# Kernel optimization log

Hardware: AMD Instinct MI355X
Metric: run time of the kernel (lower is better)

The kernel has to match this reference:

```python
import jax, jax.numpy as jnp
import numpy as np

B, L, C, H, W = 2, 4, 128, 48, 176
RATIO, DS = 0.4, 4.0   # voxel_size[0], downsample_rate
NUM_ITER = 2


def _make_pairwise_t(key):
    k1, k2 = jax.random.split(key)
    theta = jax.random.uniform(k1, (B, L, L), minval=-0.2, maxval=0.2)
    t = jax.random.uniform(k2, (B, L, L, 2), minval=-8.0, maxval=8.0)  # meters
    c, s = jnp.cos(theta), jnp.sin(theta)
    T = jnp.zeros((B, L, L, 4, 4), dtype=jnp.float32)
    T = T.at[..., 0, 0].set(c).at[..., 0, 1].set(-s)
    T = T.at[..., 1, 0].set(s).at[..., 1, 1].set(c)
    T = T.at[..., 0, 3].set(t[..., 0]).at[..., 1, 3].set(t[..., 1])
    T = T.at[..., 2, 2].set(1.0).at[..., 3, 3].set(1.0)
    d = jnp.arange(L)
    T = T.at[:, d, d].set(jnp.eye(4, dtype=jnp.float32))  # self-transform = identity
    return T


def setup_inputs():
    key = jax.random.key(0)
    ks = jax.random.split(key, 8)
    x = jax.random.normal(ks[0], (B, L, C, H, W), dtype=jnp.float32)
    record_len = jnp.array([L, L - 1], dtype=jnp.int32)
    mask = (jnp.arange(L)[None, :] < record_len[:, None]).astype(jnp.float32)
    pairwise_t_matrix = _make_pairwise_t(ks[1])
    W_msg = jax.random.normal(ks[2], (C, 2 * C, 3, 3), dtype=jnp.float32) * 0.021
    b_msg = jnp.zeros((C,), dtype=jnp.float32)
    W_gates = jax.random.normal(ks[3], (2 * C, 3 * C, 3, 3), dtype=jnp.float32) * 0.017
    b_gates = jnp.zeros((2 * C,), dtype=jnp.float32)
    W_can = jax.random.normal(ks[4], (C, 3 * C, 3, 3), dtype=jnp.float32) * 0.017
    b_can = jnp.zeros((C,), dtype=jnp.float32)
    W_mlp = jax.random.normal(ks[5], (C, C), dtype=jnp.float32) * 0.088
    b_mlp = jnp.zeros((C,), dtype=jnp.float32)
    return {"x": x, "mask": mask, "pairwise_t_matrix": pairwise_t_matrix,
            "record_len": record_len, "W_msg": W_msg, "b_msg": b_msg,
            "W_gates": W_gates, "b_gates": b_gates, "W_can": W_can,
            "b_can": b_can, "W_mlp": W_mlp, "b_mlp": b_mlp}


def _conv2d(x, w, b):
    y = jax.lax.conv_general_dilated(x, w, (1, 1), 'SAME',
                                     dimension_numbers=('NCHW', 'OIHW', 'NCHW'))
    return y + b[None, :, None, None]


def _affine_inv(T):
    # T: (..., 4, 4) neighbor->ego transform. Returns (..., 2, 3) inverse pixel
    # affine (maps dst pixel -> src pixel), i.e. get_discretized_transformation_matrix
    # + rotation-about-center + translation, then inverted (kornia warp_affine semantics).
    R = T[..., :2, :2]
    t = T[..., :2, 3] / (RATIO * DS)             # translation in pixels
    c = jnp.array([W / 2.0, H / 2.0], dtype=T.dtype)
    full_t = c - jnp.einsum('...ij,j->...i', R, c) + t   # (..., 2)
    det = R[..., 0, 0] * R[..., 1, 1] - R[..., 0, 1] * R[..., 1, 0]
    Rinv = jnp.stack([jnp.stack([R[..., 1, 1], -R[..., 0, 1]], -1),
                      jnp.stack([-R[..., 1, 0], R[..., 0, 0]], -1)], -2) / det[..., None, None]
    tinv = -jnp.einsum('...ij,...j->...i', Rinv, full_t)
    return jnp.concatenate([Rinv, tinv[..., None]], axis=-1)


def _warp_one(img, A):
    # img: (C, H, W); A: (2, 3) dst->src pixel map. Bilinear, zeros padding.
    ys, xs = jnp.meshgrid(jnp.arange(H, dtype=img.dtype),
                          jnp.arange(W, dtype=img.dtype), indexing='ij')
    sx = A[0, 0] * xs + A[0, 1] * ys + A[0, 2]
    sy = A[1, 0] * xs + A[1, 1] * ys + A[1, 2]
    x0 = jnp.floor(sx); y0 = jnp.floor(sy)
    wx1 = sx - x0; wy1 = sy - y0
    def gather(xi, yi):
        valid = ((xi >= 0) & (xi <= W - 1) & (yi >= 0) & (yi <= H - 1)).astype(img.dtype)
        xc = jnp.clip(xi, 0, W - 1).astype(jnp.int32)
        yc = jnp.clip(yi, 0, H - 1).astype(jnp.int32)
        return img[:, yc, xc] * valid
    return (gather(x0, y0) * (1 - wx1) * (1 - wy1)
            + gather(x0 + 1, y0) * wx1 * (1 - wy1)
            + gather(x0, y0 + 1) * (1 - wx1) * wy1
            + gather(x0 + 1, y0 + 1) * wx1 * wy1)


def _forward(x, mask, pairwise_t_matrix, record_len,
             W_msg, b_msg, W_gates, b_gates, W_can, b_can, W_mlp, b_mlp):
    # Ainv[b, j, i] warps neighbor j into ego i's frame; reorder to (b, i, j).
    Ainv = _affine_inv(pairwise_t_matrix)                      # (B, L, L, 2, 3)
    Ainv_bij = jnp.transpose(Ainv, (0, 2, 1, 3, 4)).reshape(-1, 2, 3)
    warp_v = jax.vmap(_warp_one)
    ones_img = jnp.ones((1, H, W), dtype=x.dtype)
    roi = jax.vmap(lambda A: _warp_one(ones_img, A))(Ainv_bij)  # (B*L*L, 1, H, W)
    com_mask = roi.reshape(B, L, L, 1, H, W) * mask[:, None, :, None, None, None]
    rec = record_len.astype(x.dtype)[:, None, None, None, None]
    feat = x
    for _ in range(NUM_ITER):
        nb = jnp.broadcast_to(feat[:, None], (B, L, L, C, H, W)).reshape(-1, C, H, W)
        warped = warp_v(nb, Ainv_bij).reshape(B, L, L, C, H, W)
        ego = jnp.broadcast_to(feat[:, :, None], (B, L, L, C, H, W))
        msg_in = jnp.concatenate([warped, ego], axis=3).reshape(-1, 2 * C, H, W)
        msg = _conv2d(msg_in, W_msg, b_msg).reshape(B, L, L, C, H, W) * com_mask
        agg = jnp.sum(msg, axis=2) / rec                        # mean over N valid cavs
        # ConvGRU, single layer / single step, zero-initialized hidden state
        gru_in = jnp.concatenate([feat, agg], axis=2).reshape(-1, 2 * C, H, W)
        h = jnp.zeros((B * L, C, H, W), dtype=x.dtype)
        gates = jax.nn.sigmoid(_conv2d(jnp.concatenate([gru_in, h], 1), W_gates, b_gates))
        r, u = jnp.split(gates, 2, axis=1)
        cand = jnp.tanh(_conv2d(jnp.concatenate([gru_in, r * h], 1), W_can, b_can))
        h = (1 - u) * h + u * cand
        feat = h.reshape(B, L, C, H, W)
    out = feat[:, 0]                                            # ego agent of each sample
    return jnp.einsum('bchw,oc->bohw', out, W_mlp) + b_mlp[None, :, None, None]


def reference(x, mask, pairwise_t_matrix, record_len,
              W_msg, b_msg, W_gates, b_gates, W_can, b_can, W_mlp, b_mlp):
    return _forward(x, mask, pairwise_t_matrix, record_len,
                    W_msg, b_msg, W_gates, b_gates, W_can, b_can, W_mlp, b_mlp)
```

## Files before the change

kernel.cpp:

```cpp
#include <hip/hip_runtime.h>
#include <math.h>

#define BB 2
#define LL 4
#define CC 128
#define HH 48
#define WWID 176
#define HW 8448

typedef _Float16 f16;
typedef __attribute__((ext_vector_type(8))) _Float16 f16x8;
typedef __attribute__((ext_vector_type(4))) _Float16 f16x4;
typedef __attribute__((ext_vector_type(2))) _Float16 f16x2;
typedef __attribute__((ext_vector_type(4))) float f32x4;
typedef __attribute__((ext_vector_type(4))) unsigned int u32x4;

__device__ __forceinline__ void ainv_from(const float* __restrict__ t, float* a)
{
    float R00=t[0], R01=t[1], t0=t[3];
    float R10=t[4], R11=t[5], t1=t[7];
    float tx = t0 * 0.625f;
    float ty = t1 * 0.625f;
    const float cx = WWID/2.0f, cy = HH/2.0f;
    float ftx = cx - (R00*cx + R01*cy) + tx;
    float fty = cy - (R10*cx + R11*cy) + ty;
    float det = R00*R11 - R01*R10;
    float inv = 1.0f/det;
    float i00 =  R11*inv, i01 = -R01*inv, i10 = -R10*inv, i11 = R00*inv;
    a[0]=i00; a[1]=i01; a[2]=-(i00*ftx + i01*fty);
    a[3]=i10; a[4]=i11; a[5]=-(i10*ftx + i11*fty);
}

__global__ __launch_bounds__(256)
void prep_kernel(const float* __restrict__ Wm, const float* __restrict__ Wg,
                 const float* __restrict__ Wc, const float* __restrict__ x,
                 const float* __restrict__ T, const float* __restrict__ mask,
                 f16* __restrict__ WmF, f16* __restrict__ WuF, f16* __restrict__ WcF,
                 f16* __restrict__ xT, float* __restrict__ fac)
{
    int bid = blockIdx.x;
    int tid = threadIdx.x;
    if (bid < 3456) {
        int which = bid / 1152;
        const float* src = (which==0) ? Wm : (which==1) ? Wg : Wc;
        f16* dst         = (which==0) ? WmF : (which==1) ? WuF : WcF;
        int oc_off = (which==1) ? 128 : 0;
        int stride = (which==0) ? 256 : 384;
        int idx = (bid % 1152)*256 + tid;
        int j     = idx & 7;
        int hi    = (idx >> 3) & 3;
        int l15   = (idx >> 5) & 15;
        int ocblk = (idx >> 9) & 7;
        int kq    = (idx >> 12) & 7;
        int tap   = idx >> 15;
        int oc  = ocblk*16 + l15;
        int cin = kq*32 + hi*8 + j;
        dst[idx] = (f16)src[((size_t)(oc_off+oc)*stride + cin)*9 + tap];
    } else if (bid < 3720) {
        int g = bid - 3456;
        int bl = g / 33;
        int pix = (g % 33)*256 + tid;
        const float* src = x + (size_t)bl*CC*HW + pix;
        f16* dst = xT + (size_t)bl*HW*CC + (size_t)pix*CC;
        for (int gg = 0; gg < 8; ++gg) {
            f16x8 v0, v1;
            #pragma unroll
            for (int c2 = 0; c2 < 8; ++c2) {
                v0[c2] = (f16)src[(size_t)(gg*16 + c2    )*HW];
                v1[c2] = (f16)src[(size_t)(gg*16 + 8 + c2)*HW];
            }
            *(f16x8*)(dst + gg*16    ) = v0;
            *(f16x8*)(dst + gg*16 + 8) = v1;
        }
    } else {
        int g = bid - 3720;
        int slot = g / 33;
        int pix = (g % 33)*256 + tid;
        int b = slot >> 4, l2 = (slot >> 2) & 3;
        float mk = mask[b*LL + l2];
        float a[6];
        ainv_from(T + slot*16, a);
        float gx = (float)(pix % WWID), gy = (float)(pix / WWID);
        float sx = a[0]*gx + a[1]*gy + a[2];
        float sy = a[3]*gx + a[4]*gy + a[5];
        float x0 = floorf(sx), y0 = floorf(sy);
        float wx = sx-x0, wy = sy-y0;
        int xi=(int)x0, yi=(int)y0;
        bool vx0 = xi>=0 && xi<WWID, vx1 = xi+1>=0 && xi+1<WWID;
        bool vy0 = yi>=0 && yi<HH,   vy1 = yi+1>=0 && yi+1<HH;
        float r = (vx0&&vy0?(1.f-wx)*(1.f-wy):0.f) + (vx1&&vy0?wx*(1.f-wy):0.f)
                + (vx0&&vy1?(1.f-wx)*wy:0.f)       + (vx1&&vy1?wx*wy:0.f);
        fac[(size_t)slot*HW + pix] = r*mk;
    }
}

__global__ __launch_bounds__(256,3)
void msg_conv_kernel(const f16* __restrict__ featT, const float* __restrict__ T,
                     const float* __restrict__ fac, const float* __restrict__ mask,
                     const int* __restrict__ reclen,
                     const f16* __restrict__ WmF, const float* __restrict__ bm,
                     f16* __restrict__ Pm, int n_l1)
{
    int z = blockIdx.z;
    int b = z / (n_l1*5);
    int rem = z - b*(n_l1*5);
    int l1 = rem / 5, src = rem % 5;
    if (l1 != 0 && mask[b*LL + l1] == 0.f) return;
    bool ego = (src == 4);
    int l2 = ego ? l1 : src;
    if (!ego && mask[b*LL + l2] == 0.f) return;
    bool gather = (!ego) && (l2 != l1);

    int ty = blockIdx.x / 11, tx = blockIdx.x % 11;
    int y0 = ty*8, x0 = tx*16;
    int tid = threadIdx.x;
    int wid = tid >> 6, lane = tid & 63;
    int wr = wid >> 1, wc = wid & 1;
    int l15 = lane & 15, hi = lane >> 4;

    __shared__ short lt[180*128];
    __shared__ float tw[4][192];
    __shared__ int   tof[4][192];

    const f16* in = featT + (size_t)(b*LL + l2)*HW*CC;

    if (gather) {
        float a6[6];
        ainv_from(T + ((b*LL + l2)*LL + l1)*16, a6);
        float a0=a6[0],a1=a6[1],a2=a6[2],a3=a6[3],a4=a6[4],a5=a6[5];
        for (int r = tid; r < 180; r += 256) {
            int yy = r / 18, xx = r - yy*18;
            int gy = y0 - 1 + yy, gx = x0 - 1 + xx;
            float w00=0.f,w10=0.f,w01=0.f,w11=0.f;
            int o00=0,o10=0,o01=0,o11=0;
            if (gy>=0 && gy<HH && gx>=0 && gx<WWID) {
                float sx = a0*(float)gx + a1*(float)gy + a2;
                float sy = a3*(float)gx + a4*(float)gy + a5;
                float xf = floorf(sx), yf = floorf(sy);
                float wx = sx-xf, wyv = sy-yf;
                int xi=(int)xf, yi=(int)yf;
                bool vx0=xi>=0&&xi<WWID, vx1=xi+1>=0&&xi+1<WWID;
                bool vy0=yi>=0&&yi<HH,   vy1=yi+1>=0&&yi+1<HH;
                int xc0=min(max(xi,0),WWID-1), xc1=min(max(xi+1,0),WWID-1);
                int yc0=min(max(yi,0),HH-1),   yc1=min(max(yi+1,0),HH-1);
                o00=(yc0*WWID+xc0)*CC; o10=(yc0*WWID+xc1)*CC;
                o01=(yc1*WWID+xc0)*CC; o11=(yc1*WWID+xc1)*CC;
                w00=(vx0&&vy0)?(1.f-wx)*(1.f-wyv):0.f;
                w10=(vx1&&vy0)?wx*(1.f-wyv):0.f;
                w01=(vx0&&vy1)?(1.f-wx)*wyv:0.f;
                w11=(vx1&&vy1)?wx*wyv:0.f;
            }
            tw[0][r]=w00; tw[1][r]=w10; tw[2][r]=w01; tw[3][r]=w11;
            tof[0][r]=o00; tof[1][r]=o10; tof[2][r]=o01; tof[3][r]=o11;
        }
        __syncthreads();
        for (int i = tid; i < 180*16; i += 256) {
            int row = i >> 4, cg = i & 15;
            f16 h00=(f16)tw[0][row], h10=(f16)tw[1][row];
            f16 h01=(f16)tw[2][row], h11=(f16)tw[3][row];
            f16x2 W00={h00,h00}, W10={h10,h10}, W01={h01,h01}, W11={h11,h11};
            int o00=tof[0][row], o10=tof[1][row], o01=tof[2][row], o11=tof[3][row];
            f16x8 t00 = *(const f16x8*)(in + o00 + cg*8);
            f16x8 t10 = *(const f16x8*)(in + o10 + cg*8);
            f16x8 t01 = *(const f16x8*)(in + o01 + cg*8);
            f16x8 t11 = *(const f16x8*)(in + o11 + cg*8);
            const f16x2* p00 = (const f16x2*)&t00;
            const f16x2* p10 = (const f16x2*)&t10;
            const f16x2* p01 = (const f16x2*)&t01;
            const f16x2* p11 = (const f16x2*)&t11;
            f16x8 outv;
            f16x2* po = (f16x2*)&outv;
            #pragma unroll
            for (int q=0;q<4;++q)
                po[q] = p00[q]*W00 + p10[q]*W10 + p01[q]*W01 + p11[q]*W11;
            int byte = row*256 + ((cg*16) ^ ((row&7)<<4));
            *(f16x8*)((char*)lt + byte) = outv;
        }
    } else {
        for (int i = tid; i < 180*16; i += 256) {
            int row = i >> 4, cg = i & 15;
            int yy = row / 18, xx = row - yy*18;
            int gy = y0 - 1 + yy, gx = x0 - 1 + xx;
            u32x4 val = {0,0,0,0};
            if (gy>=0 && gy<HH && gx>=0 && gx<WWID)
                val = *(const u32x4*)(in + (size_t)(gy*WWID+gx)*CC + cg*8);
            int byte = row*256 + ((cg*16) ^ ((row&7)<<4));
            *(u32x4*)((char*)lt + byte) = val;
        }
    }
    __syncthreads();

    f32x4 acc[4][4];
    #pragma unroll
    for (int m=0;m<4;++m)
        #pragma unroll
        for (int n=0;n<4;++n) acc[m][n] = (f32x4){0.f,0.f,0.f,0.f};

    const int kqbase = ego ? 4 : 0;
    const f16* wlane = WmF + l15*32 + hi*8;
    __builtin_amdgcn_s_setprio(1);
    for (int tap=0; tap<9; ++tap) {
        int dy = tap/3, dx = tap - dy*3;
        #pragma unroll
        for (int kk=0; kk<4; ++kk) {
            const f16* wt = wlane + (size_t)(((tap*8 + kqbase + kk)*8 + wr*4))*512;
            f16x8 av[4];
            #pragma unroll
            for (int m=0;m<4;++m)
                av[m] = *(const f16x8*)(wt + m*512);
            f16x8 bv[4];
            #pragma unroll
            for (int n=0;n<4;++n) {
                int pos = (wc*4 + n + dy)*18 + dx + l15;
                int byte = pos*256 + ((kk*64 + hi*16) ^ ((pos&7)<<4));
                bv[n] = *(const f16x8*)((const char*)lt + byte);
            }
            #pragma unroll
            for (int m=0;m<4;++m)
                #pragma unroll
                for (int n=0;n<4;++n)
                    acc[m][n] = __builtin_amdgcn_mfma_f32_16x16x32_f16(
                        av[m], bv[n], acc[m][n], 0, 0, 0);
        }
    }
    __builtin_amdgcn_s_setprio(0);

    float invrec = 1.0f / (float)reclen[b];
    float fsc[4];
    if (ego) {
        #pragma unroll
        for (int n=0;n<4;++n) fsc[n] = 0.f;
        for (int j=0;j<LL;++j) {
            if (mask[b*LL + j] == 0.f) continue;
            const float* fp = fac + (size_t)(b*16 + j*4 + l1)*HW;
            #pragma unroll
            for (int n=0;n<4;++n)
                fsc[n] += fp[(y0 + wc*4 + n)*WWID + x0 + l15];
        }
    } else {
        const float* fp = fac + (size_t)(b*16 + l2*4 + l1)*HW;
        #pragma unroll
        for (int n=0;n<4;++n)
            fsc[n] = fp[(y0 + wc*4 + n)*WWID + x0 + l15];
    }
    #pragma unroll
    for (int n=0;n<4;++n) fsc[n] *= invrec;

    f16* outp = Pm + (size_t)z*HW*CC;
    #pragma unroll
    for (int m=0;m<4;++m) {
        f32x4 b4 = {0.f,0.f,0.f,0.f};
        if (ego) b4 = *(const f32x4*)(bm + wr*64 + m*16 + hi*4);
        #pragma unroll
        for (int n=0;n<4;++n) {
            int pix = (y0 + wc*4 + n)*WWID + x0 + l15;
            int oc  = wr*64 + m*16 + hi*4;
            f32x4 v = (acc[m][n] + b4) * fsc[n];
            f16x4 h = {(f16)v[0], (f16)v[1], (f16)v[2], (f16)v[3]};
            *(f16x4*)(outp + (size_t)pix*CC + oc) = h;
        }
    }
}

__global__ __launch_bounds__(256)
void reduce_agg_kernel(const f16* __restrict__ Pm, const float* __restrict__ mask,
                       f16* __restrict__ aggT, int n_l1)
{
    int zi = blockIdx.y;
    int b = zi / n_l1, l1 = zi % n_l1;
    if (l1 != 0 && mask[b*LL + l1] == 0.f) return;
    int pix = blockIdx.x*256 + threadIdx.x;
    bool act[4];
    #pragma unroll
    for (int j=0;j<LL;++j) act[j] = (mask[b*LL + j] != 0.f);
    const f16* base = Pm + (size_t)(zi*5)*HW*CC + (size_t)pix*CC;
    f16* dst = aggT + (size_t)zi*HW*CC + (size_t)pix*CC;
    for (int cg=0; cg<16; ++cg) {
        float s[8];
        f16x8 e = *(const f16x8*)(base + (size_t)4*HW*CC + cg*8);
        #pragma unroll
        for (int j8=0;j8<8;++j8) s[j8] = (float)e[j8];
        #pragma unroll
        for (int j=0;j<4;++j) {
            if (!act[j]) continue;
            f16x8 p = *(const f16x8*)(base + (size_t)j*HW*CC + cg*8);
            #pragma unroll
            for (int j8=0;j8<8;++j8) s[j8] += (float)p[j8];
        }
        f16x8 o;
        #pragma unroll
        for (int j8=0;j8<8;++j8) o[j8] = (f16)s[j8];
        *(f16x8*)(dst + cg*8) = o;
    }
}

__global__ __launch_bounds__(256,3)
void gru_conv_kernel(const f16* __restrict__ featT, const f16* __restrict__ aggT,
                     const float* __restrict__ mask,
                     const f16* __restrict__ WuF, const f16* __restrict__ WcF,
                     f16* __restrict__ Pg, int n_l1)
{
    int z = blockIdx.z;
    int b = z / n_l1, l1 = z % n_l1;
    if (l1 != 0 && mask[b*LL + l1] == 0.f) return;
    int gate = blockIdx.y;

    int ty = blockIdx.x / 11, tx = blockIdx.x % 11;
    int y0 = ty*8, x0 = tx*16;
    int tid = threadIdx.x;
    int wid = tid >> 6, lane = tid & 63;
    int wr = wid >> 1, wc = wid & 1;
    int l15 = lane & 15, hi = lane >> 4;

    __shared__ short lt[180*128];

    f32x4 acc[4][4];
    #pragma unroll
    for (int m=0;m<4;++m)
        #pragma unroll
        for (int n=0;n<4;++n) acc[m][n] = (f32x4){0.f,0.f,0.f,0.f};

    const f16* WF = (gate==0) ? WuF : WcF;
    const f16* wlane = WF + l15*32 + hi*8;

    for (int s = 0; s < 2; ++s) {
        const f16* in = (s==0) ? featT + (size_t)(b*LL + l1)*HW*CC
                               : aggT  + (size_t)(b*n_l1 + l1)*HW*CC;
        if (s) __syncthreads();
        for (int i = tid; i < 180*16; i += 256) {
            int row = i >> 4, cg = i & 15;
            int yy = row / 18, xx = row - yy*18;
            int gy = y0 - 1 + yy, gx = x0 - 1 + xx;
            u32x4 val = {0,0,0,0};
            if (gy>=0 && gy<HH && gx>=0 && gx<WWID)
                val = *(const u32x4*)(in + (size_t)(gy*WWID+gx)*CC + cg*8);
            int byte = row*256 + ((cg*16) ^ ((row&7)<<4));
            *(u32x4*)((char*)lt + byte) = val;
        }
        __syncthreads();

        int kqbase = s*4;
        __builtin_amdgcn_s_setprio(1);
        for (int tap=0; tap<9; ++tap) {
            int dy = tap/3, dx = tap - dy*3;
            #pragma unroll
            for (int kk=0; kk<4; ++kk) {
                const f16* wt = wlane + (size_t)(((tap*8 + kqbase + kk)*8 + wr*4))*512;
                f16x8 av[4];
                #pragma unroll
                for (int m=0;m<4;++m)
                    av[m] = *(const f16x8*)(wt + m*512);
                f16x8 bv[4];
                #pragma unroll
                for (int n=0;n<4;++n) {
                    int pos = (wc*4 + n + dy)*18 + dx + l15;
                    int byte = pos*256 + ((kk*64 + hi*16) ^ ((pos&7)<<4));
                    bv[n] = *(const f16x8*)((const char*)lt + byte);
                }
                #pragma unroll
                for (int m=0;m<4;++m)
                    #pragma unroll
                    for (int n=0;n<4;++n)
                        acc[m][n] = __builtin_amdgcn_mfma_f32_16x16x32_f16(
                            av[m], bv[n], acc[m][n], 0, 0, 0);
            }
        }
        __builtin_amdgcn_s_setprio(0);
    }

    f16* outp = Pg + ((size_t)(gate*(BB*LL) + z))*HW*CC;
    #pragma unroll
    for (int m=0;m<4;++m)
        #pragma unroll
        for (int n=0;n<4;++n) {
            int pix = (y0 + wc*4 + n)*WWID + x0 + l15;
            int oc  = wr*64 + m*16 + hi*4;
            f32x4 v = acc[m][n];
            f16x4 h = {(f16)v[0], (f16)v[1], (f16)v[2], (f16)v[3]};
            *(f16x4*)(outp + (size_t)pix*CC + oc) = h;
        }
}

__global__ __launch_bounds__(256)
void combine_kernel(const f16* __restrict__ Pg, const float* __restrict__ mask,
                    const float* __restrict__ bgU, const float* __restrict__ bc,
                    f16* __restrict__ outT, int n_l1)
{
    int z = blockIdx.y;
    int b = z / n_l1, l1 = z % n_l1;
    if (l1 != 0 && mask[b*LL + l1] == 0.f) return;
    int pix = blockIdx.x*256 + threadIdx.x;
    size_t poff = (size_t)pix*CC;
    const f16* U = Pg + ((size_t)(0*(BB*LL) + z))*HW*CC + poff;
    const f16* C = Pg + ((size_t)(1*(BB*LL) + z))*HW*CC + poff;
    f16* dst = outT + (size_t)z*HW*CC + poff;
    for (int cg=0; cg<16; ++cg) {
        f16x8 u8 = *(const f16x8*)(U + cg*8);
        f16x8 c8 = *(const f16x8*)(C + cg*8);
        f16x8 o;
        #pragma unroll
        for (int j=0; j<8; ++j) {
            float uu = (float)u8[j] + bgU[cg*8 + j];
            float cc = (float)c8[j] + bc[cg*8 + j];
            float sig = 1.f/(1.f + expf(-uu));
            o[j] = (f16)(sig * tanhf(cc));
        }
        *(f16x8*)(dst + cg*8) = o;
    }
}

__global__ __launch_bounds__(256)
void mlp_kernel(const f16* __restrict__ Pg, const float* __restrict__ bgU,
                const float* __restrict__ bc, const float* __restrict__ Wm,
                const float* __restrict__ bmlp, float* __restrict__ out)
{
    int b = blockIdx.z, oc0 = blockIdx.y*32;
    int pix = blockIdx.x*256 + threadIdx.x;
    size_t poff = (size_t)pix*CC;
    const f16* U = Pg + ((size_t)(0*(BB*LL) + b))*HW*CC + poff;
    const f16* C = Pg + ((size_t)(1*(BB*LL) + b))*HW*CC + poff;
    float acc[32];
    #pragma unroll
    for (int oc=0;oc<32;++oc) acc[oc]=0.f;
    for (int c8 = 0; c8 < 16; ++c8) {
        f16x8 u8 = *(const f16x8*)(U + c8*8);
        f16x8 g8 = *(const f16x8*)(C + c8*8);
        float f[8];
        #pragma unroll
        for (int j=0;j<8;++j) {
            float uu = (float)u8[j] + bgU[c8*8 + j];
            float cc = (float)g8[j] + bc[c8*8 + j];
            float sig = 1.f/(1.f + expf(-uu));
            f[j] = sig * tanhf(cc);
        }
        #pragma unroll
        for (int oc=0; oc<32; ++oc) {
            const float* w = Wm + (size_t)(oc0+oc)*CC + c8*8;
            #pragma unroll
            for (int j=0;j<8;++j) acc[oc] = fmaf(f[j], w[j], acc[oc]);
        }
    }
    #pragma unroll
    for (int oc=0;oc<32;++oc)
        out[((size_t)b*CC + oc0+oc)*HW + pix] = acc[oc] + bmlp[oc0+oc];
}

extern "C" void kernel_launch(void* const* d_in, const int* in_sizes, int n_in,
                              void* d_out, int out_size, void* d_ws, size_t ws_size,
                              hipStream_t stream)
{
    const float* x     = (const float*)d_in[0];
    const float* mask  = (const float*)d_in[1];
    const float* T     = (const float*)d_in[2];
    const int*   recl  = (const int*)  d_in[3];
    const float* Wmsg  = (const float*)d_in[4];
    const float* bmsg  = (const float*)d_in[5];
    const float* Wg    = (const float*)d_in[6];
    const float* bg    = (const float*)d_in[7];
    const float* Wc    = (const float*)d_in[8];
    const float* bc    = (const float*)d_in[9];
    const float* Wmlp  = (const float*)d_in[10];
    const float* bmlp  = (const float*)d_in[11];
    float* out = (float*)d_out;

    char* w = (char*)d_ws;
    f16*   xT   = (f16*)w;            w += (size_t)BB*LL*HW*CC*2;
    float* fac  = (float*)w;          w += (size_t)32*HW*4;
    f16*   WmF  = (f16*)w;            w += (size_t)9*128*256*2;
    f16*   WuF  = (f16*)w;            w += (size_t)9*128*256*2;
    f16*   WcF  = (f16*)w;            w += (size_t)9*128*256*2;
    f16*   Pm   = (f16*)w;            w += (size_t)40*HW*CC*2;
    f16*   Pg   = (f16*)w;            w += (size_t)2*BB*LL*HW*CC*2;
    f16*   aggT = (f16*)w;            w += (size_t)BB*LL*HW*CC*2;
    f16*   f1T  = (f16*)w;            w += (size_t)BB*LL*HW*CC*2;

    prep_kernel<<<4776, 256, 0, stream>>>(Wmsg, Wg, Wc, x, T, mask,
                                          WmF, WuF, WcF, xT, fac);

    msg_conv_kernel<<<dim3(66, 1, BB*LL*5), 256, 0, stream>>>(
        xT, T, fac, mask, recl, WmF, bmsg, Pm, LL);
    reduce_agg_kernel<<<dim3(33, BB*LL), 256, 0, stream>>>(Pm, mask, aggT, LL);
    gru_conv_kernel<<<dim3(66, 2, BB*LL), 256, 0, stream>>>(
        xT, aggT, mask, WuF, WcF, Pg, LL);
    combine_kernel<<<dim3(33, BB*LL), 256, 0, stream>>>(
        Pg, mask, bg + CC, bc, f1T, LL);

    msg_conv_kernel<<<dim3(66, 1, BB*5), 256, 0, stream>>>(
        f1T, T, fac, mask, recl, WmF, bmsg, Pm, 1);
    reduce_agg_kernel<<<dim3(33, BB), 256, 0, stream>>>(Pm, mask, aggT, 1);
    gru_conv_kernel<<<dim3(66, 2, BB), 256, 0, stream>>>(
        f1T, aggT, mask, WuF, WcF, Pg, 1);

    mlp_kernel<<<dim3(33, 4, BB), 256, 0, stream>>>(
        Pg, bg + CC, bc, Wmlp, bmlp, out);
}
```

Baseline: 504.0 us.

## Split output channels across blocks in second-iteration convs and widen elementwise grids

The message and GRU conv kernels become templates on the number of output-channel tiles per wave. In the second iteration, which has only the ego agent, each block computes half the output channels, doubling the block count. This raises occupancy on a grid that would otherwise underfill the GPU, at the cost of reloading the input halo tile into shared memory twice. The reduce and combine kernels also split each pixel's 128 channels across 4 threads, giving 4x more blocks and shorter per-thread loops.

```diff
diff --git a/kernel.cpp b/kernel.cpp
--- a/kernel.cpp
+++ b/kernel.cpp
@@ -94,6 +94,7 @@
     }
 }
 
+template<int NM>
 __global__ __launch_bounds__(256,3)
 void msg_conv_kernel(const f16* __restrict__ featT, const float* __restrict__ T,
                      const float* __restrict__ fac, const float* __restrict__ mask,
@@ -110,6 +111,7 @@
     int l2 = ego ? l1 : src;
     if (!ego && mask[b*LL + l2] == 0.f) return;
     bool gather = (!ego) && (l2 != l1);
+    int och = blockIdx.y;
 
     int ty = blockIdx.x / 11, tx = blockIdx.x % 11;
     int y0 = ty*8, x0 = tx*16;
@@ -190,9 +192,9 @@
     }
     __syncthreads();
 
-    f32x4 acc[4][4];
-    #pragma unroll
-    for (int m=0;m<4;++m)
+    f32x4 acc[NM][4];
+    #pragma unroll
+    for (int m=0;m<NM;++m)
         #pragma unroll
         for (int n=0;n<4;++n) acc[m][n] = (f32x4){0.f,0.f,0.f,0.f};
 
@@ -203,10 +205,10 @@
         int dy = tap/3, dx = tap - dy*3;
         #pragma unroll
         for (int kk=0; kk<4; ++kk) {
-            const f16* wt = wlane + (size_t)(((tap*8 + kqbase + kk)*8 + wr*4))*512;
-            f16x8 av[4];
-            #pragma unroll
-            for (int m=0;m<4;++m)
+            const f16* wt = wlane + (size_t)(((tap*8 + kqbase + kk)*8 + och*4 + wr*NM))*512;
+            f16x8 av[NM];
+            #pragma unroll
+            for (int m=0;m<NM;++m)
                 av[m] = *(const f16x8*)(wt + m*512);
             f16x8 bv[4];
             #pragma unroll
@@ -216,7 +218,7 @@
                 bv[n] = *(const f16x8*)((const char*)lt + byte);
             }
             #pragma unroll
-            for (int m=0;m<4;++m)
+            for (int m=0;m<NM;++m)
                 #pragma unroll
                 for (int n=0;n<4;++n)
                     acc[m][n] = __builtin_amdgcn_mfma_f32_16x16x32_f16(
@@ -248,13 +250,13 @@
 
     f16* outp = Pm + (size_t)z*HW*CC;
     #pragma unroll
-    for (int m=0;m<4;++m) {
+    for (int m=0;m<NM;++m) {
+        int oc = (och*4 + wr*NM + m)*16 + hi*4;
         f32x4 b4 = {0.f,0.f,0.f,0.f};
-        if (ego) b4 = *(const f32x4*)(bm + wr*64 + m*16 + hi*4);
+        if (ego) b4 = *(const f32x4*)(bm + oc);
         #pragma unroll
         for (int n=0;n<4;++n) {
             int pix = (y0 + wc*4 + n)*WWID + x0 + l15;
-            int oc  = wr*64 + m*16 + hi*4;
             f32x4 v = (acc[m][n] + b4) * fsc[n];
             f16x4 h = {(f16)v[0], (f16)v[1], (f16)v[2], (f16)v[3]};
             *(f16x4*)(outp + (size_t)pix*CC + oc) = h;
@@ -269,13 +271,15 @@
     int zi = blockIdx.y;
     int b = zi / n_l1, l1 = zi % n_l1;
     if (l1 != 0 && mask[b*LL + l1] == 0.f) return;
-    int pix = blockIdx.x*256 + threadIdx.x;
+    int idx = blockIdx.x*256 + threadIdx.x;
+    int pix = idx >> 2, cgq = idx & 3;
     bool act[4];
     #pragma unroll
     for (int j=0;j<LL;++j) act[j] = (mask[b*LL + j] != 0.f);
-    const f16* base = Pm + (size_t)(zi*5)*HW*CC + (size_t)pix*CC;
-    f16* dst = aggT + (size_t)zi*HW*CC + (size_t)pix*CC;
-    for (int cg=0; cg<16; ++cg) {
+    size_t off = (size_t)pix*CC + cgq*32;
+    const f16* base = Pm + (size_t)(zi*5)*HW*CC + off;
+    f16* dst = aggT + (size_t)zi*HW*CC + off;
+    for (int cg=0; cg<4; ++cg) {
         float s[8];
         f16x8 e = *(const f16x8*)(base + (size_t)4*HW*CC + cg*8);
         #pragma unroll
@@ -294,16 +298,18 @@
     }
 }
 
+template<int NM>
 __global__ __launch_bounds__(256,3)
 void gru_conv_kernel(const f16* __restrict__ featT, const f16* __restrict__ aggT,
                      const float* __restrict__ mask,
                      const f16* __restrict__ WuF, const f16* __restrict__ WcF,
-                     f16* __restrict__ Pg, int n_l1)
+                     f16* __restrict__ Pg, int n_l1, int noc)
 {
     int z = blockIdx.z;
     int b = z / n_l1, l1 = z % n_l1;
     if (l1 != 0 && mask[b*LL + l1] == 0.f) return;
-    int gate = blockIdx.y;
+    int gate = blockIdx.y / noc;
+    int och  = blockIdx.y % noc;
 
     int ty = blockIdx.x / 11, tx = blockIdx.x % 11;
     int y0 = ty*8, x0 = tx*16;
@@ -314,9 +320,9 @@
 
     __shared__ short lt[180*128];
 
-    f32x4 acc[4][4];
-    #pragma unroll
-    for (int m=0;m<4;++m)
+    f32x4 acc[NM][4];
+    #pragma unroll
+    for (int m=0;m<NM;++m)
         #pragma unroll
         for (int n=0;n<4;++n) acc[m][n] = (f32x4){0.f,0.f,0.f,0.f};
 
@@ -345,10 +351,10 @@
             int dy = tap/3, dx = tap - dy*3;
             #pragma unroll
             for (int kk=0; kk<4; ++kk) {
-                const f16* wt = wlane + (size_t)(((tap*8 + kqbase + kk)*8 + wr*4))*512;
-                f16x8 av[4];
+                const f16* wt = wlane + (size_t)(((tap*8 + kqbase + kk)*8 + och*4 + wr*NM))*512;
+                f16x8 av[NM];
                 #pragma unroll
-                for (int m=0;m<4;++m)
+                for (int m=0;m<NM;++m)
                     av[m] = *(const f16x8*)(wt + m*512);
                 f16x8 bv[4];
                 #pragma unroll
@@ -358,7 +364,7 @@
                     bv[n] = *(const f16x8*)((const char*)lt + byte);
                 }
                 #pragma unroll
-                for (int m=0;m<4;++m)
+                for (int m=0;m<NM;++m)
                     #pragma unroll
                     for (int n=0;n<4;++n)
                         acc[m][n] = __builtin_amdgcn_mfma_f32_16x16x32_f16(
@@ -370,15 +376,16 @@
 
     f16* outp = Pg + ((size_t)(gate*(BB*LL) + z))*HW*CC;
     #pragma unroll
-    for (int m=0;m<4;++m)
+    for (int m=0;m<NM;++m) {
+        int oc = (och*4 + wr*NM + m)*16 + hi*4;
         #pragma unroll
         for (int n=0;n<4;++n) {
             int pix = (y0 + wc*4 + n)*WWID + x0 + l15;
-            int oc  = wr*64 + m*16 + hi*4;
             f32x4 v = acc[m][n];
             f16x4 h = {(f16)v[0], (f16)v[1], (f16)v[2], (f16)v[3]};
             *(f16x4*)(outp + (size_t)pix*CC + oc) = h;
         }
+    }
 }
 
 __global__ __launch_bounds__(256)
@@ -389,19 +396,20 @@
     int z = blockIdx.y;
     int b = z / n_l1, l1 = z % n_l1;
     if (l1 != 0 && mask[b*LL + l1] == 0.f) return;
-    int pix = blockIdx.x*256 + threadIdx.x;
-    size_t poff = (size_t)pix*CC;
+    int idx = blockIdx.x*256 + threadIdx.x;
+    int pix = idx >> 2, cgq = idx & 3;
+    size_t poff = (size_t)pix*CC + cgq*32;
     const f16* U = Pg + ((size_t)(0*(BB*LL) + z))*HW*CC + poff;
     const f16* C = Pg + ((size_t)(1*(BB*LL) + z))*HW*CC + poff;
     f16* dst = outT + (size_t)z*HW*CC + poff;
-    for (int cg=0; cg<16; ++cg) {
+    for (int cg=0; cg<4; ++cg) {
         f16x8 u8 = *(const f16x8*)(U + cg*8);
         f16x8 c8 = *(const f16x8*)(C + cg*8);
         f16x8 o;
         #pragma unroll
         for (int j=0; j<8; ++j) {
-            float uu = (float)u8[j] + bgU[cg*8 + j];
-            float cc = (float)c8[j] + bc[cg*8 + j];
+            float uu = (float)u8[j] + bgU[cgq*32 + cg*8 + j];
+            float cc = (float)c8[j] + bc[cgq*32 + cg*8 + j];
             float sig = 1.f/(1.f + expf(-uu));
             o[j] = (f16)(sig * tanhf(cc));
         }
@@ -477,19 +485,19 @@
     prep_kernel<<<4776, 256, 0, stream>>>(Wmsg, Wg, Wc, x, T, mask,
                                           WmF, WuF, WcF, xT, fac);
 
-    msg_conv_kernel<<<dim3(66, 1, BB*LL*5), 256, 0, stream>>>(
+    msg_conv_kernel<4><<<dim3(66, 1, BB*LL*5), 256, 0, stream>>>(
         xT, T, fac, mask, recl, WmF, bmsg, Pm, LL);
-    reduce_agg_kernel<<<dim3(33, BB*LL), 256, 0, stream>>>(Pm, mask, aggT, LL);
-    gru_conv_kernel<<<dim3(66, 2, BB*LL), 256, 0, stream>>>(
-        xT, aggT, mask, WuF, WcF, Pg, LL);
-    combine_kernel<<<dim3(33, BB*LL), 256, 0, stream>>>(
+    reduce_agg_kernel<<<dim3(132, BB*LL), 256, 0, stream>>>(Pm, mask, aggT, LL);
+    gru_conv_kernel<4><<<dim3(66, 2, BB*LL), 256, 0, stream>>>(
+        xT, aggT, mask, WuF, WcF, Pg, LL, 1);
+    combine_kernel<<<dim3(132, BB*LL), 256, 0, stream>>>(
         Pg, mask, bg + CC, bc, f1T, LL);
 
-    msg_conv_kernel<<<dim3(66, 1, BB*5), 256, 0, stream>>>(
+    msg_conv_kernel<2><<<dim3(66, 2, BB*5), 256, 0, stream>>>(
         f1T, T, fac, mask, recl, WmF, bmsg, Pm, 1);
-    reduce_agg_kernel<<<dim3(33, BB), 256, 0, stream>>>(Pm, mask, aggT, 1);
-    gru_conv_kernel<<<dim3(66, 2, BB), 256, 0, stream>>>(
-        f1T, aggT, mask, WuF, WcF, Pg, 1);
+    reduce_agg_kernel<<<dim3(132, BB), 256, 0, stream>>>(Pm, mask, aggT, 1);
+    gru_conv_kernel<2><<<dim3(66, 4, BB), 256, 0, stream>>>(
+        f1T, aggT, mask, WuF, WcF, Pg, 1, 2);
 
     mlp_kernel<<<dim3(33, 4, BB), 256, 0, stream>>>(
         Pg, bg + CC, bc, Wmlp, bmlp, out);
```

Measured after the change: 461.0 us. -8.5%, faster.
